# Optimization experiments

Measured on AMD Instinct MI355X. Metric: run time of the kernel, lower is better.

## Reference

```python
import jax, jax.numpy as jnp
import numpy as np

NUM_CLASSES = 1000
BATCH = 32768
RECALL_LO, RECALL_HI = 0.95, 1.0
LAMBDA_PAUC = 1.0
LABEL_SMOOTHING = 0.1
EPS = 1e-7


def setup_inputs() -> dict:
    key = jax.random.key(0)
    k1, k2 = jax.random.split(key)
    predictions = jax.random.normal(k1, (BATCH, NUM_CLASSES), dtype=jnp.float32)
    targets = jax.random.randint(k2, (BATCH,), 0, NUM_CLASSES, dtype=jnp.int64)
    weight = jnp.ones((NUM_CLASSES,), dtype=jnp.float32)
    return {"predictions": predictions, "targets": targets, "weight": weight}


def _per_class_pauc(scores, pos):
    # scores: [B] class probabilities; pos: [B] 0/1 float (is this class)
    order = jnp.argsort(-scores)  # descending
    s = scores[order]
    p = pos[order]
    cumpos = jnp.cumsum(p)          # tp counts over prefix
    cumneg = jnp.cumsum(1.0 - p)    # fp counts over prefix
    # handle ties: predictions >= threshold counts ALL samples with equal score,
    # i.e. take cumsum at the last index of each tie group
    neg_s = -s  # ascending
    last = jnp.searchsorted(neg_s, neg_s, side='right') - 1
    tp = cumpos[last]
    fp = cumneg[last]
    P = cumpos[-1]  # total positives (tp + fn)
    N = cumneg[-1]  # total negatives (fp + tn)
    tpr = jnp.where(P > 0, tp / jnp.where(P > 0, P, 1.0), 0.0)
    fpr = jnp.where(N > 0, fp / jnp.where(N > 0, N, 1.0), 0.0)
    mask = (tpr >= RECALL_LO) & (tpr <= RECALL_HI)
    # tpr is monotone non-decreasing along descending thresholds, so the mask
    # is contiguous; trapz over masked points == sum over adjacent masked pairs
    pair = mask[:-1] & mask[1:]
    pauc = jnp.sum(jnp.where(pair, 0.5 * (tpr[:-1] + tpr[1:]) * (fpr[1:] - fpr[:-1]), 0.0))
    return jnp.where(mask.any(), pauc, 0.0)


def reference(predictions, targets, weight):
    C = NUM_CLASSES
    probs = jax.nn.softmax(predictions, axis=1)
    onehot = jax.nn.one_hot(targets, C, dtype=predictions.dtype)
    t = (1.0 - LABEL_SMOOTHING) * onehot + LABEL_SMOOTHING / C
    class_targets = (t > 0.5).astype(predictions.dtype)  # [B, C]
    # per-class pAUC, vectorized over classes
    paucs = jax.vmap(_per_class_pauc, in_axes=(1, 1))(probs, class_targets)  # [C]
    max_pauc = RECALL_HI - RECALL_LO
    avg_p_auc = jnp.sum(paucs * weight) / (jnp.sum(weight) * max_pauc)
    log_probs = jax.nn.log_softmax(predictions, axis=1)
    ce_loss = -jnp.mean(jnp.sum(t * log_probs * weight, axis=1))
    pauc_loss = -jnp.log(avg_p_auc + EPS)
    return ce_loss + LAMBDA_PAUC * pauc_loss
```

## Files before the change

kernel.cpp:

```cpp
#include <hip/hip_runtime.h>
#include <math.h>

#define NCLS 1000
#define NB   32768
#define MAXP 128
#define MAXM 8

#define K1_BLOCKS 2048
#define K3_BLOCKS 4096

#define OFF_CE    0u
#define OFF_PAUC  16384u
#define OFF_CNT   49152u
#define OFF_ROW   53248u
#define OFF_POS   577536u
#define OFF_RTAB  1089536u
#define OFF_AUX   1121536u
#define OFF_REJ   1129536u

__device__ inline float wave_max_f(float v) {
#pragma unroll
    for (int m = 32; m >= 1; m >>= 1) v = fmaxf(v, __shfl_xor(v, m, 64));
    return v;
}
__device__ inline float wave_sum_f(float v) {
#pragma unroll
    for (int m = 32; m >= 1; m >>= 1) v += __shfl_xor(v, m, 64);
    return v;
}
__device__ inline double wave_sum_d(double v) {
#pragma unroll
    for (int m = 32; m >= 1; m >>= 1) {
        long long b = __double_as_longlong(v);
        b = __shfl_xor(b, m, 64);
        v += __longlong_as_double(b);
    }
    return v;
}

__global__ void pauc_init(int* __restrict__ cnt) {
    if (threadIdx.x < 1024) cnt[threadIdx.x] = 0;
}

__global__ __launch_bounds__(256)
void pauc_k1_rows(const float* __restrict__ pred, const int* __restrict__ tgt,
                  const float* __restrict__ w, float4* __restrict__ rowdata,
                  float* __restrict__ posScores, int* __restrict__ cnt,
                  double* __restrict__ ce_part) {
    const int lane = threadIdx.x & 63;
    const int wid  = threadIdx.x >> 6;
    const int gw   = blockIdx.x * 4 + wid;

    float4 wv[4];
    float sw_p = 0.f;
#pragma unroll
    for (int i = 0; i < 4; ++i) {
        int f = i * 64 + lane;
        if (f < 250) {
            wv[i] = reinterpret_cast<const float4*>(w)[f];
            sw_p += wv[i].x + wv[i].y + wv[i].z + wv[i].w;
        } else {
            wv[i] = make_float4(0.f, 0.f, 0.f, 0.f);
        }
    }
    const float SW = wave_sum_f(sw_p);

    double ce_acc = 0.0;
    for (int row = gw; row < NB; row += 8192) {
        const float4* rp4 = reinterpret_cast<const float4*>(pred + (size_t)row * NCLS);
        float4 v[4];
        float vmax = -3.0e38f;
#pragma unroll
        for (int i = 0; i < 4; ++i) {
            int f = i * 64 + lane;
            if (f < 250) {
                v[i] = rp4[f];
                vmax = fmaxf(vmax, fmaxf(fmaxf(v[i].x, v[i].y), fmaxf(v[i].z, v[i].w)));
            } else {
                v[i] = make_float4(0.f, 0.f, 0.f, 0.f);
            }
        }
        const float M = wave_max_f(vmax);

        float s_p = 0.f, wx_p = 0.f;
#pragma unroll
        for (int i = 0; i < 4; ++i) {
            int f = i * 64 + lane;
            if (f < 250) {
                s_p  += __expf(v[i].x - M) + __expf(v[i].y - M)
                      + __expf(v[i].z - M) + __expf(v[i].w - M);
                wx_p += wv[i].x * v[i].x + wv[i].y * v[i].y
                      + wv[i].z * v[i].z + wv[i].w * v[i].w;
            }
        }
        const float S  = wave_sum_f(s_p);
        const float WX = wave_sum_f(wx_p);

        if (lane == 0) {
            const float invS = 1.0f / S;
            const float L    = M + logf(S);
            const int   y    = tgt[row];
            const float xy   = pred[(size_t)row * NCLS + y];
            const float wy   = w[y];
            ce_acc += (double)(0.9f * wy * (xy - L) + 1e-4f * (WX - SW * L));
            rowdata[row] = make_float4(M, invS, L, 0.f);
            const int p = atomicAdd(&cnt[y], 1);
            if (p < MAXP) posScores[y * MAXP + p] = __expf(xy - M) * invS;
        }
    }

    __shared__ double sred[4];
    if (lane == 0) sred[wid] = ce_acc;
    __syncthreads();
    if (threadIdx.x == 0)
        ce_part[blockIdx.x] = sred[0] + sred[1] + sred[2] + sred[3];
}

__global__ __launch_bounds__(128)
void pauc_k2_thresh(const float* __restrict__ posScores, const int* __restrict__ cnt,
                    const float* __restrict__ w, float* __restrict__ rtab,
                    float2* __restrict__ aux, float* __restrict__ rej) {
    const int c = blockIdx.x;
    const int t = threadIdx.x;
    __shared__ float vals[MAXP];
    __shared__ float rloc[MAXM];
    __shared__ int   k0s;

    int P = cnt[c];
    if (P > MAXP) P = MAXP;
    if (t < MAXM) rloc[t] = -1.0f;
    if (t < P) vals[t] = posScores[c * MAXP + t];
    if (t == 0) {
        int k0 = 1;
        if (P > 0) {
            for (int k = 1; k <= P; ++k) {
                if ((float)k / (float)P >= 0.95f) { k0 = k; break; }
            }
        }
        k0s = k0;
    }
    __syncthreads();

    if (P == 0) {
        if (t == 0) { rej[c] = -3.0e38f; aux[c] = make_float2(0.f, 0.f); }
        if (t < MAXM) rtab[c * MAXM + t] = -1.0f;
        return;
    }
    const int k0 = k0s;

    if (t < P) {
        const float v = vals[t];
        int rank = 0;
        for (int u = 0; u < P; ++u) {
            const float vu = vals[u];
            rank += (vu > v) ? 1 : ((vu == v && u < t) ? 1 : 0);
        }
        const int idx = rank - (k0 - 1);
        if (idx >= 0 && idx < MAXM) rloc[idx] = v;
    }
    __syncthreads();

    if (t < MAXM) rtab[c * MAXM + t] = rloc[t];
    if (t == 0) {
        const float r1 = rloc[0];
        rej[c] = logf(r1) + 1e-3f;
        aux[c] = make_float2((float)(k0 - 1),
                             w[c] / ((float)P * (float)(NB - P)));
    }
}

__global__ __launch_bounds__(256)
void pauc_k3_scan(const float* __restrict__ pred, const int* __restrict__ tgt,
                  const float4* __restrict__ rowdata, const float* __restrict__ rej,
                  const float* __restrict__ rtab, const float2* __restrict__ aux,
                  double* __restrict__ pauc_part) {
    const int t = threadIdx.x;
    double acc = 0.0;

    float4 rj = make_float4(-3.0e38f, -3.0e38f, -3.0e38f, -3.0e38f);
    if (t < 250) rj = reinterpret_cast<const float4*>(rej)[t];

    for (int row = blockIdx.x; row < NB; row += K3_BLOCKS) {
        const float4 rd = rowdata[row];
        const int    y  = tgt[row];
        if (t < 250) {
            const float4 x = reinterpret_cast<const float4*>(pred + (size_t)row * NCLS)[t];
            const float M = rd.x, invS = rd.y, L = rd.z;
            const float xv[4] = {x.x, x.y, x.z, x.w};
            const float rs[4] = {rj.x, rj.y, rj.z, rj.w};
#pragma unroll
            for (int e = 0; e < 4; ++e) {
                const int c = 4 * t + e;
                if (xv[e] - L < rs[e] && c != y) {
                    const float s = __expf(xv[e] - M) * invS;
                    const float* rt = rtab + c * MAXM;
                    if (s < rt[0]) {
                        int gt = 0, eq = 0;
#pragma unroll
                        for (int i = 0; i < MAXM; ++i) {
                            const float r = rt[i];
                            gt += (r > s) ? 1 : 0;
                            eq += (r == s) ? 1 : 0;
                        }
                        const float2 a = aux[c];
                        acc += (double)((a.x + (float)gt + 0.5f * (float)eq) * a.y);
                    }
                }
            }
        }
    }

    acc = wave_sum_d(acc);
    __shared__ double sred[4];
    if ((threadIdx.x & 63) == 0) sred[threadIdx.x >> 6] = acc;
    __syncthreads();
    if (threadIdx.x == 0)
        pauc_part[blockIdx.x] = sred[0] + sred[1] + sred[2] + sred[3];
}

__global__ __launch_bounds__(256)
void pauc_k4_final(const double* __restrict__ ce_part, const double* __restrict__ pauc_part,
                   const float* __restrict__ w, float* __restrict__ out) {
    const int t = threadIdx.x;
    double ce = 0.0, pa = 0.0, sw = 0.0;
    for (int i = t; i < K1_BLOCKS; i += 256) ce += ce_part[i];
    for (int i = t; i < K3_BLOCKS; i += 256) pa += pauc_part[i];
    for (int i = t; i < NCLS;      i += 256) sw += (double)w[i];
    ce = wave_sum_d(ce); pa = wave_sum_d(pa); sw = wave_sum_d(sw);
    __shared__ double sc[4], sp[4], ss[4];
    const int lane = t & 63, wid = t >> 6;
    if (lane == 0) { sc[wid] = ce; sp[wid] = pa; ss[wid] = sw; }
    __syncthreads();
    if (t == 0) {
        const double ceS = sc[0] + sc[1] + sc[2] + sc[3];
        const double paS = sp[0] + sp[1] + sp[2] + sp[3];
        const double swS = ss[0] + ss[1] + ss[2] + ss[3];
        const double ce_loss = -ceS / (double)NB;
        const double avg     = paS / (swS * (1.0 - 0.95));
        out[0] = (float)(ce_loss - log(avg + 1e-7));
    }
}

extern "C" void kernel_launch(void* const* d_in, const int* in_sizes, int n_in,
                              void* d_out, int out_size, void* d_ws, size_t ws_size,
                              hipStream_t stream) {
    const float* pred = (const float*)d_in[0];
    const int*   tgt  = (const int*)d_in[1];
    const float* w    = (const float*)d_in[2];

    char* ws = (char*)d_ws;
    double* ce_part   = (double*)(ws + OFF_CE);
    double* pauc_part = (double*)(ws + OFF_PAUC);
    int*    cnt       = (int*)   (ws + OFF_CNT);
    float4* rowdata   = (float4*)(ws + OFF_ROW);
    float*  posScores = (float*) (ws + OFF_POS);
    float*  rtab      = (float*) (ws + OFF_RTAB);
    float2* aux       = (float2*)(ws + OFF_AUX);
    float*  rej       = (float*) (ws + OFF_REJ);

    pauc_init<<<1, 1024, 0, stream>>>(cnt);
    pauc_k1_rows<<<K1_BLOCKS, 256, 0, stream>>>(pred, tgt, w, rowdata, posScores, cnt, ce_part);
    pauc_k2_thresh<<<NCLS, 128, 0, stream>>>(posScores, cnt, w, rtab, aux, rej);
    pauc_k3_scan<<<K3_BLOCKS, 256, 0, stream>>>(pred, tgt, rowdata, rej, rtab, aux, pauc_part);
    pauc_k4_final<<<1, 256, 0, stream>>>(ce_part, pauc_part, w, (float*)d_out);
}
```

Before: 274.6 us.

## Fuse final reduction into scan kernel and pack per-class threshold table

```diff
diff --git a/kernel.cpp b/kernel.cpp
--- a/kernel.cpp
+++ b/kernel.cpp
@@ -4,7 +4,7 @@
 #define NCLS 1000
 #define NB   32768
 #define MAXP 128
-#define MAXM 8
+#define MAXM 4
 
 #define K1_BLOCKS 2048
 #define K3_BLOCKS 4096
@@ -14,9 +14,9 @@
 #define OFF_CNT   49152u
 #define OFF_ROW   53248u
 #define OFF_POS   577536u
-#define OFF_RTAB  1089536u
-#define OFF_AUX   1121536u
-#define OFF_REJ   1129536u
+#define OFF_PTA   1089536u
+#define OFF_PTB   1105536u
+#define OFF_REJ   1113536u
 
 __device__ inline float wave_max_f(float v) {
 #pragma unroll
@@ -36,10 +36,6 @@
         v += __longlong_as_double(b);
     }
     return v;
-}
-
-__global__ void pauc_init(int* __restrict__ cnt) {
-    if (threadIdx.x < 1024) cnt[threadIdx.x] = 0;
 }
 
 __global__ __launch_bounds__(256)
@@ -118,8 +114,8 @@
 
 __global__ __launch_bounds__(128)
 void pauc_k2_thresh(const float* __restrict__ posScores, const int* __restrict__ cnt,
-                    const float* __restrict__ w, float* __restrict__ rtab,
-                    float2* __restrict__ aux, float* __restrict__ rej) {
+                    const float* __restrict__ w, float4* __restrict__ ptabA,
+                    float2* __restrict__ ptabB, float* __restrict__ rej) {
     const int c = blockIdx.x;
     const int t = threadIdx.x;
     __shared__ float vals[MAXP];
@@ -142,8 +138,11 @@
     __syncthreads();
 
     if (P == 0) {
-        if (t == 0) { rej[c] = -3.0e38f; aux[c] = make_float2(0.f, 0.f); }
-        if (t < MAXM) rtab[c * MAXM + t] = -1.0f;
+        if (t == 0) {
+            rej[c]   = -3.0e38f;
+            ptabA[c] = make_float4(-1.f, -1.f, -1.f, -1.f);
+            ptabB[c] = make_float2(0.f, 0.f);
+        }
         return;
     }
     const int k0 = k0s;
@@ -160,20 +159,22 @@
     }
     __syncthreads();
 
-    if (t < MAXM) rtab[c * MAXM + t] = rloc[t];
     if (t == 0) {
-        const float r1 = rloc[0];
-        rej[c] = logf(r1) + 1e-3f;
-        aux[c] = make_float2((float)(k0 - 1),
-                             w[c] / ((float)P * (float)(NB - P)));
+        const float r0 = rloc[0];
+        rej[c]   = logf(r0) + 1e-3f;
+        ptabA[c] = make_float4(rloc[0], rloc[1], rloc[2], rloc[3]);
+        ptabB[c] = make_float2((float)(k0 - 1),
+                               w[c] / ((float)P * (float)(NB - P)));
     }
 }
 
 __global__ __launch_bounds__(256)
 void pauc_k3_scan(const float* __restrict__ pred, const int* __restrict__ tgt,
                   const float4* __restrict__ rowdata, const float* __restrict__ rej,
-                  const float* __restrict__ rtab, const float2* __restrict__ aux,
-                  double* __restrict__ pauc_part) {
+                  const float4* __restrict__ ptabA, const float2* __restrict__ ptabB,
+                  const float* __restrict__ w,
+                  double* __restrict__ ce_part, double* __restrict__ pauc_part,
+                  int* __restrict__ done, float* __restrict__ out) {
     const int t = threadIdx.x;
     double acc = 0.0;
 
@@ -193,17 +194,16 @@
                 const int c = 4 * t + e;
                 if (xv[e] - L < rs[e] && c != y) {
                     const float s = __expf(xv[e] - M) * invS;
-                    const float* rt = rtab + c * MAXM;
-                    if (s < rt[0]) {
-                        int gt = 0, eq = 0;
-#pragma unroll
-                        for (int i = 0; i < MAXM; ++i) {
-                            const float r = rt[i];
-                            gt += (r > s) ? 1 : 0;
-                            eq += (r == s) ? 1 : 0;
-                        }
-                        const float2 a = aux[c];
-                        acc += (double)((a.x + (float)gt + 0.5f * (float)eq) * a.y);
+                    const float4 rt = ptabA[c];
+                    if (s < rt.x) {
+                        const float gt = 1.0f + (rt.y > s ? 1.f : 0.f)
+                                              + (rt.z > s ? 1.f : 0.f)
+                                              + (rt.w > s ? 1.f : 0.f);
+                        const float eq = (rt.y == s ? 1.f : 0.f)
+                                       + (rt.z == s ? 1.f : 0.f)
+                                       + (rt.w == s ? 1.f : 0.f);
+                        const float2 a = ptabB[c];
+                        acc += (double)((a.x + gt + 0.5f * eq) * a.y);
                     }
                 }
             }
@@ -212,32 +212,36 @@
 
     acc = wave_sum_d(acc);
     __shared__ double sred[4];
-    if ((threadIdx.x & 63) == 0) sred[threadIdx.x >> 6] = acc;
-    __syncthreads();
-    if (threadIdx.x == 0)
+    __shared__ int lastFlag;
+    if ((t & 63) == 0) sred[t >> 6] = acc;
+    __syncthreads();
+    if (t == 0) {
         pauc_part[blockIdx.x] = sred[0] + sred[1] + sred[2] + sred[3];
-}
-
-__global__ __launch_bounds__(256)
-void pauc_k4_final(const double* __restrict__ ce_part, const double* __restrict__ pauc_part,
-                   const float* __restrict__ w, float* __restrict__ out) {
-    const int t = threadIdx.x;
-    double ce = 0.0, pa = 0.0, sw = 0.0;
-    for (int i = t; i < K1_BLOCKS; i += 256) ce += ce_part[i];
-    for (int i = t; i < K3_BLOCKS; i += 256) pa += pauc_part[i];
-    for (int i = t; i < NCLS;      i += 256) sw += (double)w[i];
-    ce = wave_sum_d(ce); pa = wave_sum_d(pa); sw = wave_sum_d(sw);
-    __shared__ double sc[4], sp[4], ss[4];
-    const int lane = t & 63, wid = t >> 6;
-    if (lane == 0) { sc[wid] = ce; sp[wid] = pa; ss[wid] = sw; }
-    __syncthreads();
-    if (t == 0) {
-        const double ceS = sc[0] + sc[1] + sc[2] + sc[3];
-        const double paS = sp[0] + sp[1] + sp[2] + sp[3];
-        const double swS = ss[0] + ss[1] + ss[2] + ss[3];
-        const double ce_loss = -ceS / (double)NB;
-        const double avg     = paS / (swS * (1.0 - 0.95));
-        out[0] = (float)(ce_loss - log(avg + 1e-7));
+        __threadfence();
+        const int d = atomicAdd(done, 1);
+        lastFlag = (d == K3_BLOCKS - 1) ? 1 : 0;
+    }
+    __syncthreads();
+
+    if (lastFlag) {
+        __threadfence();
+        double ce = 0.0, pa = 0.0, sw = 0.0;
+        for (int i = t; i < K1_BLOCKS; i += 256) ce += ce_part[i];
+        for (int i = t; i < K3_BLOCKS; i += 256) pa += pauc_part[i];
+        for (int i = t; i < NCLS;      i += 256) sw += (double)w[i];
+        ce = wave_sum_d(ce); pa = wave_sum_d(pa); sw = wave_sum_d(sw);
+        __shared__ double sc[4], sp[4], ss[4];
+        const int lane = t & 63, wid = t >> 6;
+        if (lane == 0) { sc[wid] = ce; sp[wid] = pa; ss[wid] = sw; }
+        __syncthreads();
+        if (t == 0) {
+            const double ceS = sc[0] + sc[1] + sc[2] + sc[3];
+            const double paS = sp[0] + sp[1] + sp[2] + sp[3];
+            const double swS = ss[0] + ss[1] + ss[2] + ss[3];
+            const double ce_loss = -ceS / (double)NB;
+            const double avg     = paS / (swS * (1.0 - 0.95));
+            out[0] = (float)(ce_loss - log(avg + 1e-7));
+        }
     }
 }
 
@@ -254,13 +258,14 @@
     int*    cnt       = (int*)   (ws + OFF_CNT);
     float4* rowdata   = (float4*)(ws + OFF_ROW);
     float*  posScores = (float*) (ws + OFF_POS);
-    float*  rtab      = (float*) (ws + OFF_RTAB);
-    float2* aux       = (float2*)(ws + OFF_AUX);
+    float4* ptabA     = (float4*)(ws + OFF_PTA);
+    float2* ptabB     = (float2*)(ws + OFF_PTB);
     float*  rej       = (float*) (ws + OFF_REJ);
-
-    pauc_init<<<1, 1024, 0, stream>>>(cnt);
+    int*    done      = cnt + 1023;
+
+    hipMemsetAsync(cnt, 0, 4096, stream);
     pauc_k1_rows<<<K1_BLOCKS, 256, 0, stream>>>(pred, tgt, w, rowdata, posScores, cnt, ce_part);
-    pauc_k2_thresh<<<NCLS, 128, 0, stream>>>(posScores, cnt, w, rtab, aux, rej);
-    pauc_k3_scan<<<K3_BLOCKS, 256, 0, stream>>>(pred, tgt, rowdata, rej, rtab, aux, pauc_part);
-    pauc_k4_final<<<1, 256, 0, stream>>>(ce_part, pauc_part, w, (float*)d_out);
-}
+    pauc_k2_thresh<<<NCLS, 128, 0, stream>>>(posScores, cnt, w, ptabA, ptabB, rej);
+    pauc_k3_scan<<<K3_BLOCKS, 256, 0, stream>>>(pred, tgt, rowdata, rej, ptabA, ptabB, w,
+                                                ce_part, pauc_part, done, (float*)d_out);
+}
```

New measurement: 343.1 us. 1.25x slower.

## Stage pAUC threshold tables in LDS as SoA and batch rows per block

Applied to the files above, without the earlier changes.

```diff
diff --git a/kernel.cpp b/kernel.cpp
--- a/kernel.cpp
+++ b/kernel.cpp
@@ -4,29 +4,41 @@
 #define NCLS 1000
 #define NB   32768
 #define MAXP 128
-#define MAXM 8
+#define MAXM 4
 
 #define K1_BLOCKS 2048
-#define K3_BLOCKS 4096
+#define K3_BLOCKS 1024
+#define ROWS_K3   32
+#define TSTRIDE   1124
 
 #define OFF_CE    0u
 #define OFF_PAUC  16384u
-#define OFF_CNT   49152u
-#define OFF_ROW   53248u
-#define OFF_POS   577536u
-#define OFF_RTAB  1089536u
-#define OFF_AUX   1121536u
-#define OFF_REJ   1129536u
-
-__device__ inline float wave_max_f(float v) {
-#pragma unroll
-    for (int m = 32; m >= 1; m >>= 1) v = fmaxf(v, __shfl_xor(v, m, 64));
-    return v;
-}
+#define OFF_CNT   24576u
+#define OFF_ROW   28672u
+#define OFF_POS   552960u
+#define OFF_SOA   1064960u
+#define OFF_REJ   1088960u
+
 __device__ inline float wave_sum_f(float v) {
 #pragma unroll
     for (int m = 32; m >= 1; m >>= 1) v += __shfl_xor(v, m, 64);
     return v;
+}
+__device__ inline void wave_max2(float& a, float& b) {
+#pragma unroll
+    for (int m = 32; m >= 1; m >>= 1) {
+        a = fmaxf(a, __shfl_xor(a, m, 64));
+        b = fmaxf(b, __shfl_xor(b, m, 64));
+    }
+}
+__device__ inline void wave_sum4(float& a, float& b, float& c, float& d) {
+#pragma unroll
+    for (int m = 32; m >= 1; m >>= 1) {
+        a += __shfl_xor(a, m, 64);
+        b += __shfl_xor(b, m, 64);
+        c += __shfl_xor(c, m, 64);
+        d += __shfl_xor(d, m, 64);
+    }
 }
 __device__ inline double wave_sum_d(double v) {
 #pragma unroll
@@ -36,10 +48,6 @@
         v += __longlong_as_double(b);
     }
     return v;
-}
-
-__global__ void pauc_init(int* __restrict__ cnt) {
-    if (threadIdx.x < 1024) cnt[threadIdx.x] = 0;
 }
 
 __global__ __launch_bounds__(256)
@@ -66,46 +74,66 @@
     const float SW = wave_sum_f(sw_p);
 
     double ce_acc = 0.0;
-    for (int row = gw; row < NB; row += 8192) {
-        const float4* rp4 = reinterpret_cast<const float4*>(pred + (size_t)row * NCLS);
-        float4 v[4];
-        float vmax = -3.0e38f;
+#pragma unroll
+    for (int pair = 0; pair < 2; ++pair) {
+        const int ra = gw * 4 + pair * 2;
+        const int rb = ra + 1;
+        const int ya = tgt[ra];
+        const int yb = tgt[rb];
+        const float4* pa = reinterpret_cast<const float4*>(pred + (size_t)ra * NCLS);
+        const float4* pb = reinterpret_cast<const float4*>(pred + (size_t)rb * NCLS);
+
+        float4 va[4], vb[4];
+        float ma = -3.0e38f, mb = -3.0e38f;
 #pragma unroll
         for (int i = 0; i < 4; ++i) {
             int f = i * 64 + lane;
             if (f < 250) {
-                v[i] = rp4[f];
-                vmax = fmaxf(vmax, fmaxf(fmaxf(v[i].x, v[i].y), fmaxf(v[i].z, v[i].w)));
+                va[i] = pa[f];
+                vb[i] = pb[f];
+                ma = fmaxf(ma, fmaxf(fmaxf(va[i].x, va[i].y), fmaxf(va[i].z, va[i].w)));
+                mb = fmaxf(mb, fmaxf(fmaxf(vb[i].x, vb[i].y), fmaxf(vb[i].z, vb[i].w)));
             } else {
-                v[i] = make_float4(0.f, 0.f, 0.f, 0.f);
+                va[i] = make_float4(0.f, 0.f, 0.f, 0.f);
+                vb[i] = make_float4(0.f, 0.f, 0.f, 0.f);
             }
         }
-        const float M = wave_max_f(vmax);
-
-        float s_p = 0.f, wx_p = 0.f;
+        wave_max2(ma, mb);
+
+        float sa = 0.f, wxa = 0.f, sb = 0.f, wxb = 0.f;
 #pragma unroll
         for (int i = 0; i < 4; ++i) {
             int f = i * 64 + lane;
             if (f < 250) {
-                s_p  += __expf(v[i].x - M) + __expf(v[i].y - M)
-                      + __expf(v[i].z - M) + __expf(v[i].w - M);
-                wx_p += wv[i].x * v[i].x + wv[i].y * v[i].y
-                      + wv[i].z * v[i].z + wv[i].w * v[i].w;
+                sa  += __expf(va[i].x - ma) + __expf(va[i].y - ma)
+                     + __expf(va[i].z - ma) + __expf(va[i].w - ma);
+                wxa += wv[i].x * va[i].x + wv[i].y * va[i].y
+                     + wv[i].z * va[i].z + wv[i].w * va[i].w;
+                sb  += __expf(vb[i].x - mb) + __expf(vb[i].y - mb)
+                     + __expf(vb[i].z - mb) + __expf(vb[i].w - mb);
+                wxb += wv[i].x * vb[i].x + wv[i].y * vb[i].y
+                     + wv[i].z * vb[i].z + wv[i].w * vb[i].w;
             }
         }
-        const float S  = wave_sum_f(s_p);
-        const float WX = wave_sum_f(wx_p);
+        wave_sum4(sa, wxa, sb, wxb);
 
         if (lane == 0) {
-            const float invS = 1.0f / S;
-            const float L    = M + logf(S);
-            const int   y    = tgt[row];
-            const float xy   = pred[(size_t)row * NCLS + y];
-            const float wy   = w[y];
-            ce_acc += (double)(0.9f * wy * (xy - L) + 1e-4f * (WX - SW * L));
-            rowdata[row] = make_float4(M, invS, L, 0.f);
-            const int p = atomicAdd(&cnt[y], 1);
-            if (p < MAXP) posScores[y * MAXP + p] = __expf(xy - M) * invS;
+            const float invSa = 1.0f / sa;
+            const float La    = ma + logf(sa);
+            const float invSb = 1.0f / sb;
+            const float Lb    = mb + logf(sb);
+            const float xya   = pred[(size_t)ra * NCLS + ya];
+            const float xyb   = pred[(size_t)rb * NCLS + yb];
+            const float wya   = w[ya];
+            const float wyb   = w[yb];
+            ce_acc += (double)(0.9f * wya * (xya - La) + 1e-4f * (wxa - SW * La));
+            ce_acc += (double)(0.9f * wyb * (xyb - Lb) + 1e-4f * (wxb - SW * Lb));
+            rowdata[ra] = make_float4(ma, invSa, La, 0.f);
+            rowdata[rb] = make_float4(mb, invSb, Lb, 0.f);
+            const int p_a = atomicAdd(&cnt[ya], 1);
+            if (p_a < MAXP) posScores[ya * MAXP + p_a] = __expf(xya - ma) * invSa;
+            const int p_b = atomicAdd(&cnt[yb], 1);
+            if (p_b < MAXP) posScores[yb * MAXP + p_b] = __expf(xyb - mb) * invSb;
         }
     }
 
@@ -118,8 +146,8 @@
 
 __global__ __launch_bounds__(128)
 void pauc_k2_thresh(const float* __restrict__ posScores, const int* __restrict__ cnt,
-                    const float* __restrict__ w, float* __restrict__ rtab,
-                    float2* __restrict__ aux, float* __restrict__ rej) {
+                    const float* __restrict__ w, float* __restrict__ soa,
+                    float* __restrict__ rej) {
     const int c = blockIdx.x;
     const int t = threadIdx.x;
     __shared__ float vals[MAXP];
@@ -142,8 +170,12 @@
     __syncthreads();
 
     if (P == 0) {
-        if (t == 0) { rej[c] = -3.0e38f; aux[c] = make_float2(0.f, 0.f); }
-        if (t < MAXM) rtab[c * MAXM + t] = -1.0f;
+        if (t == 0) {
+            rej[c] = -3.0e38f;
+            soa[0 * NCLS + c] = -1.f; soa[1 * NCLS + c] = -1.f;
+            soa[2 * NCLS + c] = -1.f; soa[3 * NCLS + c] = -1.f;
+            soa[4 * NCLS + c] = 0.f;  soa[5 * NCLS + c] = 0.f;
+        }
         return;
     }
     const int k0 = k0s;
@@ -160,61 +192,95 @@
     }
     __syncthreads();
 
-    if (t < MAXM) rtab[c * MAXM + t] = rloc[t];
     if (t == 0) {
-        const float r1 = rloc[0];
-        rej[c] = logf(r1) + 1e-3f;
-        aux[c] = make_float2((float)(k0 - 1),
-                             w[c] / ((float)P * (float)(NB - P)));
+        const float r0 = rloc[0];
+        rej[c] = logf(r0) + 1e-3f;
+        soa[0 * NCLS + c] = rloc[0];
+        soa[1 * NCLS + c] = rloc[1];
+        soa[2 * NCLS + c] = rloc[2];
+        soa[3 * NCLS + c] = rloc[3];
+        soa[4 * NCLS + c] = (float)(k0 - 1);
+        soa[5 * NCLS + c] = w[c] / ((float)P * (float)(NB - P));
     }
 }
 
 __global__ __launch_bounds__(256)
 void pauc_k3_scan(const float* __restrict__ pred, const int* __restrict__ tgt,
                   const float4* __restrict__ rowdata, const float* __restrict__ rej,
-                  const float* __restrict__ rtab, const float2* __restrict__ aux,
-                  double* __restrict__ pauc_part) {
+                  const float* __restrict__ soa, double* __restrict__ pauc_part) {
+    __shared__ float tab[6 * TSTRIDE];
     const int t = threadIdx.x;
-    double acc = 0.0;
+
+#pragma unroll
+    for (int f = 0; f < 6; ++f)
+        for (int i = t; i < NCLS; i += 256)
+            tab[f * TSTRIDE + i + (i >> 3)] = soa[f * NCLS + i];
 
     float4 rj = make_float4(-3.0e38f, -3.0e38f, -3.0e38f, -3.0e38f);
     if (t < 250) rj = reinterpret_cast<const float4*>(rej)[t];
-
-    for (int row = blockIdx.x; row < NB; row += K3_BLOCKS) {
-        const float4 rd = rowdata[row];
-        const int    y  = tgt[row];
+    __syncthreads();
+
+    double acc = 0.0;
+    const int rbase = blockIdx.x * ROWS_K3;
+
+    for (int j = 0; j < ROWS_K3; j += 4) {
+        const int r = rbase + j;
+        float4 x0, x1, x2, x3;
         if (t < 250) {
-            const float4 x = reinterpret_cast<const float4*>(pred + (size_t)row * NCLS)[t];
-            const float M = rd.x, invS = rd.y, L = rd.z;
-            const float xv[4] = {x.x, x.y, x.z, x.w};
+            const float4* p = reinterpret_cast<const float4*>(pred + (size_t)r * NCLS);
+            x0 = p[t];
+            x1 = p[250 + t];
+            x2 = p[500 + t];
+            x3 = p[750 + t];
+        }
+        const float4 rd0 = rowdata[r],     rd1 = rowdata[r + 1];
+        const float4 rd2 = rowdata[r + 2], rd3 = rowdata[r + 3];
+        const int y0 = tgt[r],     y1 = tgt[r + 1];
+        const int y2 = tgt[r + 2], y3 = tgt[r + 3];
+
+        if (t < 250) {
             const float rs[4] = {rj.x, rj.y, rj.z, rj.w};
-#pragma unroll
-            for (int e = 0; e < 4; ++e) {
-                const int c = 4 * t + e;
-                if (xv[e] - L < rs[e] && c != y) {
-                    const float s = __expf(xv[e] - M) * invS;
-                    const float* rt = rtab + c * MAXM;
-                    if (s < rt[0]) {
-                        int gt = 0, eq = 0;
-#pragma unroll
-                        for (int i = 0; i < MAXM; ++i) {
-                            const float r = rt[i];
-                            gt += (r > s) ? 1 : 0;
-                            eq += (r == s) ? 1 : 0;
-                        }
-                        const float2 a = aux[c];
-                        acc += (double)((a.x + (float)gt + 0.5f * (float)eq) * a.y);
-                    }
-                }
+#define PROC(X, RD, Y)                                                          \
+            {                                                                   \
+                const float M = RD.x, invS = RD.y, L = RD.z;                    \
+                const float xv[4] = {X.x, X.y, X.z, X.w};                       \
+                _Pragma("unroll")                                               \
+                for (int e = 0; e < 4; ++e) {                                   \
+                    const int c = 4 * t + e;                                    \
+                    if (xv[e] - L < rs[e] && c != (Y)) {                        \
+                        const float s = __expf(xv[e] - M) * invS;               \
+                        const int sc = c + (c >> 3);                            \
+                        const float r0v = tab[sc];                              \
+                        if (s < r0v) {                                          \
+                            const float r1v = tab[1 * TSTRIDE + sc];            \
+                            const float r2v = tab[2 * TSTRIDE + sc];            \
+                            const float r3v = tab[3 * TSTRIDE + sc];            \
+                            const float bse = tab[4 * TSTRIDE + sc];            \
+                            const float cof = tab[5 * TSTRIDE + sc];            \
+                            const float gt = 1.0f + (r1v > s ? 1.f : 0.f)       \
+                                                  + (r2v > s ? 1.f : 0.f)       \
+                                                  + (r3v > s ? 1.f : 0.f);      \
+                            const float eq = (r1v == s ? 1.f : 0.f)             \
+                                           + (r2v == s ? 1.f : 0.f)             \
+                                           + (r3v == s ? 1.f : 0.f);            \
+                            acc += (double)((bse + gt + 0.5f * eq) * cof);      \
+                        }                                                       \
+                    }                                                           \
+                }                                                               \
             }
+            PROC(x0, rd0, y0)
+            PROC(x1, rd1, y1)
+            PROC(x2, rd2, y2)
+            PROC(x3, rd3, y3)
+#undef PROC
         }
     }
 
     acc = wave_sum_d(acc);
     __shared__ double sred[4];
-    if ((threadIdx.x & 63) == 0) sred[threadIdx.x >> 6] = acc;
-    __syncthreads();
-    if (threadIdx.x == 0)
+    if ((t & 63) == 0) sred[t >> 6] = acc;
+    __syncthreads();
+    if (t == 0)
         pauc_part[blockIdx.x] = sred[0] + sred[1] + sred[2] + sred[3];
 }
 
@@ -254,13 +320,12 @@
     int*    cnt       = (int*)   (ws + OFF_CNT);
     float4* rowdata   = (float4*)(ws + OFF_ROW);
     float*  posScores = (float*) (ws + OFF_POS);
-    float*  rtab      = (float*) (ws + OFF_RTAB);
-    float2* aux       = (float2*)(ws + OFF_AUX);
+    float*  soa       = (float*) (ws + OFF_SOA);
     float*  rej       = (float*) (ws + OFF_REJ);
 
-    pauc_init<<<1, 1024, 0, stream>>>(cnt);
+    hipMemsetAsync(cnt, 0, 4096, stream);
     pauc_k1_rows<<<K1_BLOCKS, 256, 0, stream>>>(pred, tgt, w, rowdata, posScores, cnt, ce_part);
-    pauc_k2_thresh<<<NCLS, 128, 0, stream>>>(posScores, cnt, w, rtab, aux, rej);
-    pauc_k3_scan<<<K3_BLOCKS, 256, 0, stream>>>(pred, tgt, rowdata, rej, rtab, aux, pauc_part);
+    pauc_k2_thresh<<<NCLS, 128, 0, stream>>>(posScores, cnt, w, soa, rej);
+    pauc_k3_scan<<<K3_BLOCKS, 256, 0, stream>>>(pred, tgt, rowdata, rej, soa, pauc_part);
     pauc_k4_final<<<1, 256, 0, stream>>>(ce_part, pauc_part, w, (float*)d_out);
 }
```

Result: faster. 243.8 us (-11.2%).
